# Optimization experiments

Hardware: AMD Instinct MI355X
Metric: run time of the kernel (lower is better)

Reference implementation:

```python
import jax, jax.numpy as jnp
import numpy as np

B, N, DIN, DOUT = 8, 2048, 512, 256
NUM_BUCKETS = 20


def setup_inputs() -> dict:
    key = jax.random.key(0)
    ks = jax.random.split(key, 12)
    s_in = 1.0 / np.sqrt(DIN)
    s_out = 1.0 / np.sqrt(DOUT)
    return {
        "x": jax.random.normal(ks[0], (B, N, DIN), dtype=jnp.float32),
        "price_rank": jax.random.randint(ks[1], (B, N), 0, N, dtype=jnp.int64),
        "Wq": jax.random.uniform(ks[2], (DOUT, DIN), jnp.float32, -s_in, s_in),
        "bq": jax.random.uniform(ks[3], (DOUT,), jnp.float32, -s_in, s_in),
        "Wk": jax.random.uniform(ks[4], (DOUT, DIN), jnp.float32, -s_in, s_in),
        "bk": jax.random.uniform(ks[5], (DOUT,), jnp.float32, -s_in, s_in),
        "Wv": jax.random.uniform(ks[6], (DOUT, DIN), jnp.float32, -s_in, s_in),
        "bv": jax.random.uniform(ks[7], (DOUT,), jnp.float32, -s_in, s_in),
        "Ws": jax.random.uniform(ks[8], (1, DOUT), jnp.float32, -s_out, s_out),
        "bs": jax.random.uniform(ks[9], (1,), jnp.float32, -s_out, s_out),
        "rank_emb": jax.random.normal(ks[10], (NUM_BUCKETS, 1), dtype=jnp.float32),
        "rank_w": jnp.ones((1,), dtype=jnp.float32),
    }


def reference(x, price_rank, Wq, bq, Wk, bk, Wv, bv, Ws, bs, rank_emb, rank_w):
    scale = jnp.sqrt(jnp.asarray(DOUT, dtype=x.dtype))
    q = jnp.einsum("bnd,od->bno", x, Wq) + bq  # [B,N,DOUT]
    k = jnp.einsum("bnd,od->bno", x, Wk) + bk
    v = jnp.einsum("bnd,od->bno", x, Wv) + bv
    scores = jnp.einsum("bno,bmo->bnm", q, k) / scale  # [B,N,N]
    # learned pairwise rank-distance bias gate
    rank_dist = jnp.abs(price_rank[:, :, None] - price_rank[:, None, :])
    buckets = jnp.clip(rank_dist // 5, 0, NUM_BUCKETS - 1)  # [B,N,N] int
    prior = rank_emb[buckets, 0]  # gather embedding, squeeze last dim
    gate = jax.nn.sigmoid(rank_w[0] * prior)
    scores = scores * gate
    attn = jax.nn.softmax(scores, axis=2)
    context = jnp.einsum("bnm,bmo->bno", attn, v)  # [B,N,DOUT]
    winner = jax.nn.sigmoid(jnp.einsum("bno,uo->bnu", context, Ws) + bs)[..., 0]
    return winner  # [B,N]
```

## Files before the change

kernel.cpp:

```cpp
#include <hip/hip_runtime.h>
#include <hip/hip_bf16.h>

#define B_    8
#define N_    2048
#define DIN_  512
#define DOUT_ 256
#define NBUCK 20

typedef __attribute__((ext_vector_type(8))) short  short8;
typedef __attribute__((ext_vector_type(4))) float  floatx4;

__device__ __forceinline__ unsigned short f2b(float f) {
    __hip_bfloat16 h = __float2bfloat16(f);
    unsigned short u;
    __builtin_memcpy(&u, &h, 2);
    return u;
}

__device__ __forceinline__ void load_lds16(const unsigned short* g, unsigned short* l) {
    __builtin_amdgcn_global_load_lds(
        (const __attribute__((address_space(1))) unsigned int*)g,
        (__attribute__((address_space(3))) unsigned int*)l, 16, 0, 0);
}

__device__ __forceinline__ float fexp2(float x) {
    float r;
    asm("v_exp_f32 %0, %1" : "=v"(r) : "v"(x));
    return r;
}

__global__ __launch_bounds__(256) void prep_kernel(
    const float* __restrict__ Wv, const float* __restrict__ Ws,
    const float* __restrict__ bv,
    float* __restrict__ wvs, float* __restrict__ bvs) {
    const int blk = blockIdx.x, tid = threadIdx.x;
    __shared__ float wsl[DOUT_];
    wsl[tid] = Ws[tid];
    __syncthreads();
    if (tid < 128) {
        int d = blk * 128 + tid;
        float s0 = 0.f, s1 = 0.f, s2 = 0.f, s3 = 0.f;
#pragma unroll 8
        for (int o = 0; o < DOUT_; o += 4) {
            s0 += Wv[(size_t)(o + 0) * DIN_ + d] * wsl[o + 0];
            s1 += Wv[(size_t)(o + 1) * DIN_ + d] * wsl[o + 1];
            s2 += Wv[(size_t)(o + 2) * DIN_ + d] * wsl[o + 2];
            s3 += Wv[(size_t)(o + 3) * DIN_ + d] * wsl[o + 3];
        }
        wvs[d] = (s0 + s1) + (s2 + s3);
    }
    if (blk == 0 && tid < 64) {
        float bb = wsl[tid] * bv[tid] + wsl[tid + 64] * bv[tid + 64] +
                   wsl[tid + 128] * bv[tid + 128] + wsl[tid + 192] * bv[tid + 192];
        for (int off = 1; off < 64; off <<= 1) bb += __shfl_xor(bb, off, 64);
        if (tid == 0) *bvs = bb;
    }
}

__global__ __launch_bounds__(256) void cvt_x_kernel(const float* __restrict__ x,
                                                    const float* __restrict__ wvs,
                                                    const float* __restrict__ bvs,
                                                    const float* __restrict__ wq,
                                                    const float* __restrict__ wk,
                                                    unsigned short* __restrict__ xb,
                                                    unsigned short* __restrict__ wdst,
                                                    float* __restrict__ vw) {
    int tid = threadIdx.x;
    if (blockIdx.x >= 4096) {
        int i = ((blockIdx.x - 4096) * 256 + tid) * 8;
        const float* src = (i < 131072) ? (wq + i) : (wk + (i - 131072));
        float4 a = *(const float4*)(src);
        float4 b = *(const float4*)(src + 4);
        uint4 r;
        r.x = f2b(a.x) | ((unsigned)f2b(a.y) << 16);
        r.y = f2b(a.z) | ((unsigned)f2b(a.w) << 16);
        r.z = f2b(b.x) | ((unsigned)f2b(b.y) << 16);
        r.w = f2b(b.z) | ((unsigned)f2b(b.w) << 16);
        *(uint4*)(wdst + i) = r;
        return;
    }
    int wave = tid >> 6, lane = tid & 63;
    int row = blockIdx.x * 4 + wave;
    size_t base = (size_t)row * DIN_ + lane * 8;
    float4 a = *(const float4*)(x + base);
    float4 b = *(const float4*)(x + base + 4);
    float4 wa = *(const float4*)(wvs + lane * 8);
    float4 wb = *(const float4*)(wvs + lane * 8 + 4);
    uint4 r;
    r.x = f2b(a.x) | ((unsigned)f2b(a.y) << 16);
    r.y = f2b(a.z) | ((unsigned)f2b(a.w) << 16);
    r.z = f2b(b.x) | ((unsigned)f2b(b.y) << 16);
    r.w = f2b(b.z) | ((unsigned)f2b(b.w) << 16);
    *(uint4*)(xb + base) = r;
    float d = a.x * wa.x + a.y * wa.y + a.z * wa.z + a.w * wa.w +
              b.x * wb.x + b.y * wb.y + b.z * wb.z + b.w * wb.w;
    for (int off = 1; off < 64; off <<= 1) d += __shfl_xor(d, off, 64);
    if (lane == 0) vw[row] = d + *bvs;
}

__global__ __launch_bounds__(256, 2) void qkv_kernel(
    const unsigned short* __restrict__ xb, const unsigned short* __restrict__ wb,
    const float* __restrict__ bq, const float* __restrict__ bk,
    unsigned short* __restrict__ qo, unsigned short* __restrict__ ko) {
    __shared__ unsigned short alds[2][128 * 64];
    __shared__ unsigned short blds[2][128 * 64];
    const int g = blockIdx.x;
    const int xcd = g & 7, t2 = g >> 3;
    const int colBlk = t2 & 3, rowGrp = t2 >> 2;
    const int rowBlk = rowGrp * 8 + xcd;
    const int tid = threadIdx.x;
    const int wave = tid >> 6, lane = tid & 63, quad = lane >> 4, l16 = lane & 15;
    const int wr = wave >> 1, wc = wave & 1;
    const int row0 = rowBlk * 128, col0 = colBlk * 128;
    const int sw3 = l16 & 7;

    floatx4 acc[4][4];
#pragma unroll
    for (int i = 0; i < 4; ++i)
#pragma unroll
        for (int j = 0; j < 4; ++j) acc[i][j] = (floatx4){0.f, 0.f, 0.f, 0.f};

    const int gseg = (lane & 7) ^ (lane >> 3);
    const unsigned short* ag = xb + (size_t)(row0 + wave * 8 + (lane >> 3)) * DIN_ + gseg * 8;
    const unsigned short* bg = wb + (size_t)(col0 + wave * 8 + (lane >> 3)) * DIN_ + gseg * 8;

#pragma unroll
    for (int i = 0; i < 4; ++i) {
        load_lds16(ag + (size_t)i * 32 * DIN_, &alds[0][wave * 512 + i * 2048]);
        load_lds16(bg + (size_t)i * 32 * DIN_, &blds[0][wave * 512 + i * 2048]);
    }
    __syncthreads();

#pragma unroll 1
    for (int t = 0; t < 8; ++t) {
        const unsigned short* al = (t & 1) ? alds[1] : alds[0];
        const unsigned short* bl = (t & 1) ? blds[1] : blds[0];
        unsigned short* aln = (t & 1) ? &alds[0][0] : &alds[1][0];
        unsigned short* bln = (t & 1) ? &blds[0][0] : &blds[1][0];
        if (t < 7) {
            size_t koff = (size_t)(t + 1) * 64;
#pragma unroll
            for (int i = 0; i < 4; ++i) {
                load_lds16(ag + (size_t)i * 32 * DIN_ + koff, aln + wave * 512 + i * 2048);
                load_lds16(bg + (size_t)i * 32 * DIN_ + koff, bln + wave * 512 + i * 2048);
            }
        }
#pragma unroll
        for (int h = 0; h < 2; ++h) {
            short8 af[4], bf[4];
#pragma unroll
            for (int f = 0; f < 4; ++f) {
                int ar = wr * 64 + f * 16 + l16;
                int br = wc * 64 + f * 16 + l16;
                int s  = (h * 4 + quad) ^ sw3;
                af[f] = *(const short8*)&al[(size_t)ar * 64 + s * 8];
                bf[f] = *(const short8*)&bl[(size_t)br * 64 + s * 8];
            }
#pragma unroll
            for (int i = 0; i < 4; ++i)
#pragma unroll
                for (int j = 0; j < 4; ++j)
                    acc[i][j] = __builtin_amdgcn_mfma_f32_16x16x32_bf16(af[i], bf[j], acc[i][j], 0, 0, 0);
        }
        __syncthreads();
    }

#pragma unroll
    for (int j = 0; j < 4; ++j) {
        int col = col0 + wc * 64 + j * 16 + l16;
        unsigned short* dst = (col < 256) ? qo : ko;
        float bias = (col < 256) ? bq[col] : bk[col - 256];
        int c = col & 255;
#pragma unroll
        for (int i = 0; i < 4; ++i)
#pragma unroll
            for (int r = 0; r < 4; ++r) {
                int row = row0 + wr * 64 + i * 16 + quad * 4 + r;
                dst[(size_t)row * DOUT_ + c] = f2b(acc[i][j][r] + bias);
            }
    }
}

__global__ __launch_bounds__(512, 1) void attn_kernel(
    const unsigned short* __restrict__ q, const unsigned short* __restrict__ k,
    const float* __restrict__ vw, const int* __restrict__ pr,
    const float* __restrict__ rank_emb, const float* __restrict__ rank_w,
    const float* __restrict__ bs, float* __restrict__ out) {
    const int g = blockIdx.x;
    const int b = g & 7, rblk = g >> 3;
    const int tid = threadIdx.x, wave = tid >> 6, lane = tid & 63;
    const int quad = lane >> 4, l16 = lane & 15;
    const int n0 = rblk * 64;
    const int l8 = lane & 7;

    __shared__ unsigned short kbuf[2][32768];
    __shared__ float gtab_r[NBUCK * 8];
    __shared__ float lL[8][64], wdL[8][64];

    if (tid < NBUCK * 8)
        gtab_r[tid] = 0.0625f * 1.44269504f /
                      (1.f + __expf(-rank_w[0] * rank_emb[tid >> 3]));

    const unsigned short* qb = q + (size_t)b * N_ * DOUT_;
    const unsigned short* kb = k + (size_t)b * N_ * DOUT_;
    const float* vwb = vw + b * N_;
    const int* prb = pr + b * N_;

    short8 qf[4][8];
#pragma unroll
    for (int a = 0; a < 4; ++a)
#pragma unroll
        for (int c = 0; c < 8; ++c)
            qf[a][c] = *(const short8*)(qb + (size_t)(n0 + a * 16 + l16) * DOUT_ + c * 32 + quad * 8);

    float prn5[4][4];
#pragma unroll
    for (int a = 0; a < 4; ++a)
#pragma unroll
        for (int r = 0; r < 4; ++r)
            prn5[a][r] = (float)prb[n0 + a * 16 + quad * 4 + r] * 0.2f;

    float lacc[4][4], wacc[4][4];
#pragma unroll
    for (int a = 0; a < 4; ++a)
#pragma unroll
        for (int r = 0; r < 4; ++r) { lacc[a][r] = 0.f; wacc[a][r] = 0.f; }

    const int stg_rbase = wave * 2 + (lane >> 5);
    const int stg_gseg  = (lane & 31) ^ (stg_rbase & 7);
    const unsigned short* stg_src0 = kb + (size_t)stg_rbase * DOUT_ + stg_gseg * 8;
    unsigned short* sdst0 = &kbuf[0][wave * 512];
    unsigned short* sdst1 = &kbuf[1][wave * 512];

    auto stage = [&](int j, unsigned short* sdst) {
        const unsigned short* src = stg_src0 + (size_t)j * 128 * DOUT_;
#pragma unroll
        for (int i = 0; i < 8; ++i)
            load_lds16(src + (size_t)i * 4096, sdst + i * 4096);
    };
    auto mfma = [&](floatx4 (&s)[4], const unsigned short* buf) {
#pragma unroll
        for (int a = 0; a < 4; ++a) s[a] = (floatx4){0.f, 0.f, 0.f, 0.f};
        __builtin_amdgcn_s_setprio(1);
#pragma unroll
        for (int c = 0; c < 8; ++c) {
            int seg = (c * 4 + quad) ^ l8;
            short8 kf = *(const short8*)&buf[(size_t)(wave * 16 + l16) * 256 + seg * 8];
            s[0] = __builtin_amdgcn_mfma_f32_16x16x32_bf16(qf[0][c], kf, s[0], 0, 0, 0);
            s[1] = __builtin_amdgcn_mfma_f32_16x16x32_bf16(qf[1][c], kf, s[1], 0, 0, 0);
            s[2] = __builtin_amdgcn_mfma_f32_16x16x32_bf16(qf[2][c], kf, s[2], 0, 0, 0);
            s[3] = __builtin_amdgcn_mfma_f32_16x16x32_bf16(qf[3][c], kf, s[3], 0, 0, 0);
        }
        __builtin_amdgcn_s_setprio(0);
    };
    auto gate = [&](floatx4 (&s)[4], int pm, float w) {
        float pm5 = (float)pm * 0.2f;
#pragma unroll
        for (int a = 0; a < 4; ++a)
#pragma unroll
            for (int r = 0; r < 4; ++r) {
                float d = fabsf(prn5[a][r] - pm5);
                int idx = (int)fminf(d, 19.0f);
                float p = fexp2(s[a][r] * gtab_r[idx * 8 + l8]);
                lacc[a][r] += p;
                wacc[a][r] += p * w;
            }
    };

    floatx4 sA[4], sB[4];
    const int colq = wave * 16 + l16;

    stage(0, sdst0);
    int   pmA = prb[colq];
    float wA  = vwb[colq];
    __syncthreads();
    stage(1, sdst1);
    int   pmB = prb[128 + colq];
    float wB  = vwb[128 + colq];
    mfma(sA, kbuf[0]);
    __syncthreads();

#pragma unroll 1
    for (int jj = 0; jj < 7; ++jj) {
        {
            int jn = 2 * jj + 2;
            stage(jn, sdst0);
            int   p0 = prb[jn * 128 + colq];
            float w0 = vwb[jn * 128 + colq];
            mfma(sB, kbuf[1]);
            __builtin_amdgcn_sched_barrier(0);
            gate(sA, pmA, wA);
            pmA = p0; wA = w0;
            __syncthreads();
        }
        {
            int jn = 2 * jj + 3;
            stage(jn, sdst1);
            int   p0 = prb[jn * 128 + colq];
            float w0 = vwb[jn * 128 + colq];
            mfma(sA, kbuf[0]);
            __builtin_amdgcn_sched_barrier(0);
            gate(sB, pmB, wB);
            pmB = p0; wB = w0;
            __syncthreads();
        }
    }
    mfma(sB, kbuf[1]);
    __builtin_amdgcn_sched_barrier(0);
    gate(sA, pmA, wA);
    gate(sB, pmB, wB);

#pragma unroll
    for (int off = 1; off < 16; off <<= 1) {
#pragma unroll
        for (int a = 0; a < 4; ++a)
#pragma unroll
            for (int r = 0; r < 4; ++r) {
                lacc[a][r] += __shfl_xor(lacc[a][r], off, 64);
                wacc[a][r] += __shfl_xor(wacc[a][r], off, 64);
            }
    }
    if (l16 == 0) {
#pragma unroll
        for (int a = 0; a < 4; ++a)
#pragma unroll
            for (int r = 0; r < 4; ++r) {
                int row = a * 16 + quad * 4 + r;
                lL[wave][row]  = lacc[a][r];
                wdL[wave][row] = wacc[a][r];
            }
    }
    __syncthreads();
    if (tid < 64) {
        float l = 0.f, wd = 0.f;
#pragma unroll
        for (int s2 = 0; s2 < 8; ++s2) { l += lL[s2][tid]; wd += wdL[s2][tid]; }
        float logit = wd / l + bs[0];
        out[(size_t)b * N_ + n0 + tid] = 1.f / (1.f + __expf(-logit));
    }
}

extern "C" void kernel_launch(void* const* d_in, const int* in_sizes, int n_in,
                              void* d_out, int out_size, void* d_ws, size_t ws_size,
                              hipStream_t stream) {
    const float* x   = (const float*)d_in[0];
    const int*   pr  = (const int*)d_in[1];
    const float* Wq  = (const float*)d_in[2];
    const float* bq  = (const float*)d_in[3];
    const float* Wk  = (const float*)d_in[4];
    const float* bk  = (const float*)d_in[5];
    const float* Wv  = (const float*)d_in[6];
    const float* bv  = (const float*)d_in[7];
    const float* Ws  = (const float*)d_in[8];
    const float* bs  = (const float*)d_in[9];
    const float* remb = (const float*)d_in[10];
    const float* rw   = (const float*)d_in[11];
    float* out = (float*)d_out;

    char* ws = (char*)d_ws;
    unsigned short* xb  = (unsigned short*)ws;
    unsigned short* wb  = (unsigned short*)(ws + 16777216);
    unsigned short* q   = (unsigned short*)(ws + 17301504);
    unsigned short* kk  = (unsigned short*)(ws + 25690112);
    float*          vwp = (float*)(ws + 34078720);
    float*          wvs = (float*)(ws + 34144256);
    float*          bvs = (float*)(ws + 34146304);

    hipLaunchKernelGGL(prep_kernel, dim3(4), dim3(256), 0, stream,
                       Wv, Ws, bv, wvs, bvs);
    hipLaunchKernelGGL(cvt_x_kernel, dim3(4224), dim3(256), 0, stream,
                       x, wvs, bvs, Wq, Wk, xb, wb, vwp);
    hipLaunchKernelGGL(qkv_kernel, dim3(512), dim3(256), 0, stream,
                       xb, wb, bq, bk, q, kk);
    hipLaunchKernelGGL(attn_kernel, dim3(256), dim3(512), 0, stream,
                       q, kk, vwp, pr, remb, rw, bs, out);
}
```

Baseline: 167.2 us.

## Split attention rows across 16 waves and simplify double-buffered loop

The attention kernel goes from 512 to 1024 threads per block. Waves are now arranged as two row groups of 32 query rows by eight 16-column key chunks, which halves each wave's Q fragments and accumulators. The manual two-stage A/B software pipeline, which overlapped one tile's MFMA with the previous tile's gating, is replaced by a single loop. That loop prefetches the next K tile into the other LDS buffer and relies on the extra waves to hide latency. The gate table is widened to 32 copies per bucket to spread LDS bank accesses, and the final reduction is adapted to the two row groups, at the cost of losing the explicit MFMA/VALU overlap.

```diff
diff --git a/kernel.cpp b/kernel.cpp
--- a/kernel.cpp
+++ b/kernel.cpp
@@ -181,7 +181,7 @@
     }
 }
 
-__global__ __launch_bounds__(512, 1) void attn_kernel(
+__global__ __launch_bounds__(1024) void attn_kernel(
     const unsigned short* __restrict__ q, const unsigned short* __restrict__ k,
     const float* __restrict__ vw, const int* __restrict__ pr,
     const float* __restrict__ rank_emb, const float* __restrict__ rank_w,
@@ -191,38 +191,40 @@
     const int tid = threadIdx.x, wave = tid >> 6, lane = tid & 63;
     const int quad = lane >> 4, l16 = lane & 15;
     const int n0 = rblk * 64;
-    const int l8 = lane & 7;
+    const int rg = wave >> 3, ch = wave & 7;
 
     __shared__ unsigned short kbuf[2][32768];
-    __shared__ float gtab_r[NBUCK * 8];
-    __shared__ float lL[8][64], wdL[8][64];
-
-    if (tid < NBUCK * 8)
+    __shared__ float gtab_r[NBUCK * 32];
+    __shared__ float lL[16][32], wdL[16][32];
+
+    if (tid < NBUCK * 32)
         gtab_r[tid] = 0.0625f * 1.44269504f /
-                      (1.f + __expf(-rank_w[0] * rank_emb[tid >> 3]));
+                      (1.f + __expf(-rank_w[0] * rank_emb[tid >> 5]));
 
     const unsigned short* qb = q + (size_t)b * N_ * DOUT_;
     const unsigned short* kb = k + (size_t)b * N_ * DOUT_;
     const float* vwb = vw + b * N_;
     const int* prb = pr + b * N_;
-
-    short8 qf[4][8];
-#pragma unroll
-    for (int a = 0; a < 4; ++a)
+    const int l8 = lane & 7;
+    const int l31 = lane & 31;
+
+    short8 qf[2][8];
+#pragma unroll
+    for (int a = 0; a < 2; ++a)
 #pragma unroll
         for (int c = 0; c < 8; ++c)
-            qf[a][c] = *(const short8*)(qb + (size_t)(n0 + a * 16 + l16) * DOUT_ + c * 32 + quad * 8);
-
-    float prn5[4][4];
-#pragma unroll
-    for (int a = 0; a < 4; ++a)
+            qf[a][c] = *(const short8*)(qb + (size_t)(n0 + rg * 32 + a * 16 + l16) * DOUT_ + c * 32 + quad * 8);
+
+    float prn5[2][4];
+#pragma unroll
+    for (int a = 0; a < 2; ++a)
 #pragma unroll
         for (int r = 0; r < 4; ++r)
-            prn5[a][r] = (float)prb[n0 + a * 16 + quad * 4 + r] * 0.2f;
-
-    float lacc[4][4], wacc[4][4];
-#pragma unroll
-    for (int a = 0; a < 4; ++a)
+            prn5[a][r] = (float)prb[n0 + rg * 32 + a * 16 + quad * 4 + r] * 0.2f;
+
+    float lacc[2][4], wacc[2][4];
+#pragma unroll
+    for (int a = 0; a < 2; ++a)
 #pragma unroll
         for (int r = 0; r < 4; ++r) { lacc[a][r] = 0.f; wacc[a][r] = 0.f; }
 
@@ -235,85 +237,62 @@
     auto stage = [&](int j, unsigned short* sdst) {
         const unsigned short* src = stg_src0 + (size_t)j * 128 * DOUT_;
 #pragma unroll
-        for (int i = 0; i < 8; ++i)
-            load_lds16(src + (size_t)i * 4096, sdst + i * 4096);
+        for (int i = 0; i < 4; ++i)
+            load_lds16(src + (size_t)i * 8192, sdst + i * 8192);
     };
-    auto mfma = [&](floatx4 (&s)[4], const unsigned short* buf) {
-#pragma unroll
-        for (int a = 0; a < 4; ++a) s[a] = (floatx4){0.f, 0.f, 0.f, 0.f};
+    auto mfma = [&](floatx4 (&s)[2], const unsigned short* buf) {
+#pragma unroll
+        for (int a = 0; a < 2; ++a) s[a] = (floatx4){0.f, 0.f, 0.f, 0.f};
         __builtin_amdgcn_s_setprio(1);
 #pragma unroll
         for (int c = 0; c < 8; ++c) {
             int seg = (c * 4 + quad) ^ l8;
-            short8 kf = *(const short8*)&buf[(size_t)(wave * 16 + l16) * 256 + seg * 8];
+            short8 kf = *(const short8*)&buf[(size_t)(ch * 16 + l16) * 256 + seg * 8];
             s[0] = __builtin_amdgcn_mfma_f32_16x16x32_bf16(qf[0][c], kf, s[0], 0, 0, 0);
             s[1] = __builtin_amdgcn_mfma_f32_16x16x32_bf16(qf[1][c], kf, s[1], 0, 0, 0);
-            s[2] = __builtin_amdgcn_mfma_f32_16x16x32_bf16(qf[2][c], kf, s[2], 0, 0, 0);
-            s[3] = __builtin_amdgcn_mfma_f32_16x16x32_bf16(qf[3][c], kf, s[3], 0, 0, 0);
         }
         __builtin_amdgcn_s_setprio(0);
     };
-    auto gate = [&](floatx4 (&s)[4], int pm, float w) {
+    auto gate = [&](floatx4 (&s)[2], int pm, float w) {
         float pm5 = (float)pm * 0.2f;
 #pragma unroll
-        for (int a = 0; a < 4; ++a)
+        for (int a = 0; a < 2; ++a)
 #pragma unroll
             for (int r = 0; r < 4; ++r) {
                 float d = fabsf(prn5[a][r] - pm5);
                 int idx = (int)fminf(d, 19.0f);
-                float p = fexp2(s[a][r] * gtab_r[idx * 8 + l8]);
+                float p = fexp2(s[a][r] * gtab_r[idx * 32 + l31]);
                 lacc[a][r] += p;
                 wacc[a][r] += p * w;
             }
     };
 
-    floatx4 sA[4], sB[4];
-    const int colq = wave * 16 + l16;
-
+    floatx4 s[2];
+    const int colq = ch * 16 + l16;
+
+    int   pm_cur = prb[colq];
+    float w_cur  = vwb[colq];
     stage(0, sdst0);
-    int   pmA = prb[colq];
-    float wA  = vwb[colq];
     __syncthreads();
-    stage(1, sdst1);
-    int   pmB = prb[128 + colq];
-    float wB  = vwb[128 + colq];
-    mfma(sA, kbuf[0]);
-    __syncthreads();
 
 #pragma unroll 1
-    for (int jj = 0; jj < 7; ++jj) {
-        {
-            int jn = 2 * jj + 2;
-            stage(jn, sdst0);
-            int   p0 = prb[jn * 128 + colq];
-            float w0 = vwb[jn * 128 + colq];
-            mfma(sB, kbuf[1]);
-            __builtin_amdgcn_sched_barrier(0);
-            gate(sA, pmA, wA);
-            pmA = p0; wA = w0;
-            __syncthreads();
-        }
-        {
-            int jn = 2 * jj + 3;
-            stage(jn, sdst1);
-            int   p0 = prb[jn * 128 + colq];
-            float w0 = vwb[jn * 128 + colq];
-            mfma(sA, kbuf[0]);
-            __builtin_amdgcn_sched_barrier(0);
-            gate(sB, pmB, wB);
-            pmB = p0; wB = w0;
-            __syncthreads();
-        }
-    }
-    mfma(sB, kbuf[1]);
-    __builtin_amdgcn_sched_barrier(0);
-    gate(sA, pmA, wA);
-    gate(sB, pmB, wB);
+    for (int j = 0; j < 16; ++j) {
+        const unsigned short* bufc = (j & 1) ? kbuf[1] : kbuf[0];
+        unsigned short* sdn = (j & 1) ? sdst0 : sdst1;
+        int nxt = (j < 15) ? (j + 1) : j;
+        int   pm_nxt = prb[nxt * 128 + colq];
+        float w_nxt  = vwb[nxt * 128 + colq];
+        if (j < 15) stage(j + 1, sdn);
+        mfma(s, bufc);
+        gate(s, pm_cur, w_cur);
+        pm_cur = pm_nxt; w_cur = w_nxt;
+        __syncthreads();
+    }
 
 #pragma unroll
     for (int off = 1; off < 16; off <<= 1) {
 #pragma unroll
-        for (int a = 0; a < 4; ++a)
+        for (int a = 0; a < 2; ++a)
 #pragma unroll
             for (int r = 0; r < 4; ++r) {
                 lacc[a][r] += __shfl_xor(lacc[a][r], off, 64);
@@ -322,7 +301,7 @@
     }
     if (l16 == 0) {
 #pragma unroll
-        for (int a = 0; a < 4; ++a)
+        for (int a = 0; a < 2; ++a)
 #pragma unroll
             for (int r = 0; r < 4; ++r) {
                 int row = a * 16 + quad * 4 + r;
@@ -332,9 +311,13 @@
     }
     __syncthreads();
     if (tid < 64) {
+        int rg2 = tid >> 5, sub = tid & 31;
         float l = 0.f, wd = 0.f;
 #pragma unroll
-        for (int s2 = 0; s2 < 8; ++s2) { l += lL[s2][tid]; wd += wdL[s2][tid]; }
+        for (int c2 = 0; c2 < 8; ++c2) {
+            l  += lL[rg2 * 8 + c2][sub];
+            wd += wdL[rg2 * 8 + c2][sub];
+        }
         float logit = wd / l + bs[0];
         out[(size_t)b * N_ + n0 + tid] = 1.f / (1.f + __expf(-logit));
     }
@@ -372,6 +355,6 @@
                        x, wvs, bvs, Wq, Wk, xb, wb, vwp);
     hipLaunchKernelGGL(qkv_kernel, dim3(512), dim3(256), 0, stream,
                        xb, wb, bq, bk, q, kk);
-    hipLaunchKernelGGL(attn_kernel, dim3(256), dim3(512), 0, stream,
+    hipLaunchKernelGGL(attn_kernel, dim3(256), dim3(1024), 0, stream,
                        q, kk, vwp, pr, remb, rw, bs, out);
 }
```

Measured after the change: 149.3 us. 10.7% less time.
